# Optimization experiments

Hardware: AMD Instinct MI355X
Metric: run time of the kernel (lower is better)

## Reference

```python
import jax, jax.numpy as jnp
import numpy as np

N_HEAD = 16
EPS = 1e-6


def setup_inputs() -> dict:
    key = jax.random.key(0)
    ks = jax.random.split(key, 5)
    B, T, C = 2, 2048, 1024
    hd = C // N_HEAD
    x = jax.random.normal(ks[0], (B, T, C), dtype=jnp.float32)
    # rotary frequencies (unit-magnitude complex, decomposed into cos/sin)
    theta = 10000.0 ** (-np.arange(0, hd, 2, dtype=np.float32) / hd)  # [hd/2]
    ang = np.arange(T, dtype=np.float32)[:, None] * theta[None, :]    # [T, hd/2]
    freqs_cos = jnp.asarray(np.cos(ang))
    freqs_sin = jnp.asarray(np.sin(ang))
    w_attn = jax.random.normal(ks[1], (3 * C, C), dtype=jnp.float32) * 0.02
    w_proj = jax.random.normal(ks[2], (C, C), dtype=jnp.float32) * 0.02
    q_norm_w = jnp.ones((hd,), dtype=jnp.float32)
    k_norm_w = jnp.ones((hd,), dtype=jnp.float32)
    return {"x": x, "freqs_cos": freqs_cos, "freqs_sin": freqs_sin,
            "w_attn": w_attn, "w_proj": w_proj,
            "q_norm_w": q_norm_w, "k_norm_w": k_norm_w}


def _rmsnorm(x, w):
    # x: [..., hd]; per-last-dim RMSNorm with learned scale
    rms = jax.lax.rsqrt(jnp.mean(x * x, axis=-1, keepdims=True) + EPS)
    return x * rms * w


def _rope(x, cos, sin):
    # x: [B, T, H, hd]; cos/sin: [T, hd/2] -> broadcast [1, T, 1, hd/2]
    x2 = x.reshape(*x.shape[:-1], -1, 2)  # [B,T,H,hd/2,2]
    x0, x1 = x2[..., 0], x2[..., 1]
    c = cos[None, :, None, :]
    s = sin[None, :, None, :]
    r0 = x0 * c - x1 * s
    r1 = x0 * s + x1 * c
    return jnp.stack([r0, r1], axis=-1).reshape(x.shape)


def reference(x, freqs_cos, freqs_sin, w_attn, w_proj, q_norm_w, k_norm_w):
    B, T, C = x.shape
    H = N_HEAD
    hd = C // H
    qkv = x @ w_attn.T  # [B, T, 3C]
    q, k, v = jnp.split(qkv, 3, axis=-1)
    q = q.reshape(B, T, H, hd)
    k = k.reshape(B, T, H, hd)
    v = v.reshape(B, T, H, hd)
    q = _rmsnorm(q, q_norm_w)
    k = _rmsnorm(k, k_norm_w)
    q = _rope(q, freqs_cos[:T], freqs_sin[:T])
    k = _rope(k, freqs_cos[:T], freqs_sin[:T])
    scale = 1.0 / jnp.sqrt(jnp.asarray(hd, dtype=x.dtype))
    # causal SDPA: scores [B, H, T, T]
    scores = jnp.einsum('bihd,bjhd->bhij', q, k) * scale
    causal = jnp.tril(jnp.ones((T, T), dtype=bool))
    scores = jnp.where(causal[None, None], scores, jnp.finfo(scores.dtype).min)
    p = jax.nn.softmax(scores, axis=-1)
    y = jnp.einsum('bhij,bjhd->bihd', p, v).reshape(B, T, C)
    return y @ w_proj.T
```

## Files before the change

kernel.cpp:

```cpp
#include <hip/hip_runtime.h>

typedef unsigned short u16;
typedef unsigned int u32;
typedef __bf16 bf16x8 __attribute__((ext_vector_type(8)));
typedef float f32x4 __attribute__((ext_vector_type(4)));

__device__ __forceinline__ u16 f2bf(float f) {
    union { float f; u32 u; } v;
    v.f = f;
    u32 r = v.u + 0x7fffu + ((v.u >> 16) & 1u);
    return (u16)(r >> 16);
}

__device__ __forceinline__ u32 fbits(float f) {
    union { float f; u32 u; } v; v.f = f; return v.u;
}

__device__ __forceinline__ void glds16(const void* g, void* l) {
    __builtin_amdgcn_global_load_lds(
        (__attribute__((address_space(1))) unsigned int*)(g),
        (__attribute__((address_space(3))) unsigned int*)(l), 16, 0, 0);
}

#define MFMA __builtin_amdgcn_mfma_f32_16x16x32_bf16

__global__ void castbf3(const float* __restrict__ a, u16* __restrict__ oa,
                        const float* __restrict__ b, u16* __restrict__ ob,
                        const float* __restrict__ c, u16* __restrict__ oc,
                        const float* __restrict__ fcos, const float* __restrict__ fsin,
                        float2* __restrict__ csb) {
    int blk = blockIdx.x;
    if (blk < 4096) {
        int i = blk * 256 + threadIdx.x;
        float4 v = ((const float4*)a)[i];
        ushort4 o;
        o.x = f2bf(v.x); o.y = f2bf(v.y); o.z = f2bf(v.z); o.w = f2bf(v.w);
        ((ushort4*)oa)[i] = o;
    } else if (blk < 7168) {
        int i = (blk - 4096) * 256 + threadIdx.x;
        int n = i >> 8, c4 = i & 255;
        int np;
        if (n < 2048) {
            int part = n >> 10, rem = n & 1023;
            int h = rem >> 6, d = rem & 63;
            int nd = (d >> 1) + ((d & 1) << 5);
            np = part * 1024 + h * 64 + nd;
        } else np = n;
        float4 v = ((const float4*)b)[i];
        ushort4 o;
        o.x = f2bf(v.x); o.y = f2bf(v.y); o.z = f2bf(v.z); o.w = f2bf(v.w);
        ((ushort4*)ob)[np * 256 + c4] = o;
    } else if (blk < 8192) {
        int i = (blk - 7168) * 256 + threadIdx.x;
        float4 v = ((const float4*)c)[i];
        ushort4 o;
        o.x = f2bf(v.x); o.y = f2bf(v.y); o.z = f2bf(v.z); o.w = f2bf(v.w);
        ((ushort4*)oc)[i] = o;
    } else {
        int i = (blk - 8192) * 256 + threadIdx.x;
        csb[i] = make_float2(fcos[i], fsin[i]);
    }
}

__global__ __launch_bounds__(256) void gemm_qkv(
    const u16* __restrict__ A, const u16* __restrict__ B,
    const float2* __restrict__ csb,
    const float* __restrict__ qw, const float* __restrict__ kw,
    u16* __restrict__ q, u16* __restrict__ k, u16* __restrict__ vt)
{
    __shared__ alignas(16) u16 As[128 * 32];
    __shared__ alignas(16) u16 Bs[128 * 32];
    __shared__ alignas(16) u16 Es[2 * 128 * 64];
    const int tid = threadIdx.x;
    const int lane = tid & 63;
    const int wave = tid >> 6;
    const int bm = blockIdx.y * 128, bn = blockIdx.x * 128;
    const int wm = (wave >> 1) * 64, wn = (wave & 1) * 64;
    const int ln = lane & 15, quad = lane >> 4;
    const int K = 1024;

    f32x4 acc[4][4] = {};

    const int srow = tid >> 2;
    const int scol = (tid & 3) * 8;
    const u16* gA = A + (size_t)(bm + srow) * K + scol;
    const u16* gB = B + (size_t)(bn + srow) * K + scol;
    u16* lA = &As[wave * 512];
    u16* lB = &Bs[wave * 512];

    for (int k0 = 0; k0 < K; k0 += 32) {
        glds16(gA + k0, lA);
        glds16(gA + (size_t)64 * K + k0, lA + 2048);
        glds16(gB + k0, lB);
        glds16(gB + (size_t)64 * K + k0, lB + 2048);
        __builtin_amdgcn_s_waitcnt(0);
        __syncthreads();

        bf16x8 af[4], bfr[4];
#pragma unroll
        for (int i = 0; i < 4; ++i)
            af[i] = *(const bf16x8*)&As[(wm + i * 16 + ln) * 32 + quad * 8];
#pragma unroll
        for (int j = 0; j < 4; ++j)
            bfr[j] = *(const bf16x8*)&Bs[(wn + j * 16 + ln) * 32 + quad * 8];
#pragma unroll
        for (int i = 0; i < 4; ++i)
#pragma unroll
            for (int j = 0; j < 4; ++j)
                acc[i][j] = MFMA(af[i], bfr[j], acc[i][j], 0, 0, 0);
        __syncthreads();
    }

    const int part = bn >> 10;
    const int headw = wave & 1;
    const int h0 = (bn & 1023) >> 6;
    const float SC = 0.18033688011112042f;
    const int b = bm >> 11, tbase = bm & 2047;

    if (part == 2) {
#pragma unroll
        for (int i = 0; i < 4; ++i) {
            int tlb = wm + i * 16 + quad * 4;
#pragma unroll
            for (int j = 0; j < 4; ++j) {
                int d = j * 16 + ln;
                uint2 pk;
                pk.x = __builtin_amdgcn_perm(fbits(acc[i][j][1]), fbits(acc[i][j][0]), 0x07060302u);
                pk.y = __builtin_amdgcn_perm(fbits(acc[i][j][3]), fbits(acc[i][j][2]), 0x07060302u);
                *(uint2*)&Es[headw * 8192 + d * 128 + (tlb ^ (ln << 3))] = pk;
            }
        }
        __syncthreads();
#pragma unroll
        for (int c = 0; c < 8; ++c) {
            int cid = c * 256 + tid;
            int tc = cid & 15, d = (cid >> 4) & 63, hd = cid >> 10;
            uint4 v = *(const uint4*)&Es[hd * 8192 + d * 128 + ((tc ^ (d & 15)) << 3)];
            size_t dst = ((size_t)((b * 16 + h0 + hd) * 64 + d)) * 2048
                       + tbase + ((tc >> 3) << 6) + (((tc & 7) ^ (d & 7)) << 3);
            *(uint4*)&vt[dst] = v;
        }
        return;
    }

    const float* nw = (part == 0) ? qw : kw;
    float wv[4];
#pragma unroll
    for (int j = 0; j < 4; ++j) {
        int nd = j * 16 + ln;
        int od = ((nd & 31) << 1) | (nd >> 5);
        wv[j] = nw[od];
    }

    if (part == 0) {
#pragma unroll
        for (int i = 0; i < 4; ++i) {
            float oj[4][4];
#pragma unroll
            for (int r = 0; r < 4; ++r) {
                int tloc = wm + i * 16 + quad * 4 + r;
                int t = (bm + tloc) & 2047;
                float v0 = acc[i][0][r], v1 = acc[i][1][r];
                float v2 = acc[i][2][r], v3 = acc[i][3][r];
                float ss = v0 * v0 + v1 * v1 + v2 * v2 + v3 * v3;
                ss += __shfl_xor(ss, 1);
                ss += __shfl_xor(ss, 2);
                ss += __shfl_xor(ss, 4);
                ss += __shfl_xor(ss, 8);
                float g = rsqrtf(ss * (1.0f / 64.0f) + 1e-6f) * SC;
                float x0a = v0 * g * wv[0], x0b = v1 * g * wv[1];
                float x1a = v2 * g * wv[2], x1b = v3 * g * wv[3];
                float2 cs0 = csb[t * 32 + ln];
                float2 cs1 = csb[t * 32 + 16 + ln];
                oj[0][r] = x0a * cs0.x - x1a * cs0.y;
                oj[2][r] = x0a * cs0.y + x1a * cs0.x;
                oj[1][r] = x0b * cs1.x - x1b * cs1.y;
                oj[3][r] = x0b * cs1.y + x1b * cs1.x;
            }
            int tlb = wm + i * 16 + quad * 4;
#pragma unroll
            for (int j = 0; j < 4; ++j) {
                uint2 pk;
                pk.x = __builtin_amdgcn_perm(fbits(oj[j][1]), fbits(oj[j][0]), 0x07060302u);
                pk.y = __builtin_amdgcn_perm(fbits(oj[j][3]), fbits(oj[j][2]), 0x07060302u);
                *(uint2*)&Es[headw * 8192 + (j * 16 + ln) * 128 + (tlb ^ (ln << 3))] = pk;
            }
        }
        __syncthreads();
#pragma unroll
        for (int c = 0; c < 8; ++c) {
            int cid = c * 256 + tid;
            int tc = cid & 15, d = (cid >> 4) & 63, hd = cid >> 10;
            uint4 v = *(const uint4*)&Es[hd * 8192 + d * 128 + ((tc ^ (d & 15)) << 3)];
            size_t dst = ((size_t)((b * 16 + h0 + hd) * 64 + d)) * 2048 + tbase + tc * 8;
            *(uint4*)&q[dst] = v;
        }
        return;
    }

#pragma unroll
    for (int i = 0; i < 4; ++i) {
#pragma unroll
        for (int r = 0; r < 4; ++r) {
            int tloc = wm + i * 16 + quad * 4 + r;
            int t = (bm + tloc) & 2047;

            float v0 = acc[i][0][r], v1 = acc[i][1][r];
            float v2 = acc[i][2][r], v3 = acc[i][3][r];
            float ss = v0 * v0 + v1 * v1 + v2 * v2 + v3 * v3;
            ss += __shfl_xor(ss, 1);
            ss += __shfl_xor(ss, 2);
            ss += __shfl_xor(ss, 4);
            ss += __shfl_xor(ss, 8);
            float g = rsqrtf(ss * (1.0f / 64.0f) + 1e-6f);

            float x0a = v0 * g * wv[0], x0b = v1 * g * wv[1];
            float x1a = v2 * g * wv[2], x1b = v3 * g * wv[3];
            float2 cs0 = csb[t * 32 + ln];
            float2 cs1 = csb[t * 32 + 16 + ln];
            float o0 = x0a * cs0.x - x1a * cs0.y;
            float o2 = x0a * cs0.y + x1a * cs0.x;
            float o1 = x0b * cs1.x - x1b * cs1.y;
            float o3 = x0b * cs1.y + x1b * cs1.x;

            u16* e = &Es[headw * 8192 + tloc * 64 + ln];
            e[((0 ^ quad) << 4)] = f2bf(o0);
            e[((1 ^ quad) << 4)] = f2bf(o1);
            e[((2 ^ quad) << 4)] = f2bf(o2);
            e[((3 ^ quad) << 4)] = f2bf(o3);
        }
    }
    __syncthreads();
#pragma unroll
    for (int c = 0; c < 8; ++c) {
        int cid = c * 256 + tid;
        int dc = cid & 7, tloc = (cid >> 3) & 127, hd = cid >> 10;
        int q2 = (tloc >> 2) & 3;
        int sq = (dc >> 1) ^ q2;
        uint4 v = *(const uint4*)&Es[hd * 8192 + tloc * 64 + sq * 16 + (dc & 1) * 8];
        int gm = bm + tloc;
        int bb = gm >> 11, t = gm & 2047;
        size_t rb = ((size_t)((bb * 16 + h0 + hd) * 2048 + t)) * 64;
        *(uint4*)&k[rb + ((dc ^ (t & 7)) << 3)] = v;
    }
}

__global__ __launch_bounds__(256) void gemm64(
    const u16* __restrict__ A, const u16* __restrict__ B,
    float* __restrict__ C, int M, int N, int K)
{
    __shared__ alignas(16) u16 As[64 * 32];
    __shared__ alignas(16) u16 Bs[128 * 32];
    const int tid = threadIdx.x;
    const int lane = tid & 63;
    const int wave = tid >> 6;
    const int bm = blockIdx.y * 64, bn = blockIdx.x * 128;
    const int wm = (wave >> 1) * 32, wn = (wave & 1) * 64;
    const int ln = lane & 15, quad = lane >> 4;

    f32x4 acc[2][4] = {};

    const int srow = tid >> 2;
    const int scol = (tid & 3) * 8;
    const u16* gA = A + (size_t)(bm + (srow & 63)) * K + scol;
    const u16* gB = B + (size_t)(bn + srow) * K + scol;
    u16* lA = &As[wave * 512];
    u16* lB = &Bs[wave * 512];

    for (int k0 = 0; k0 < K; k0 += 32) {
        glds16(gA + k0, lA);
        glds16(gB + k0, lB);
        glds16(gB + (size_t)64 * K + k0, lB + 2048);
        __builtin_amdgcn_s_waitcnt(0);
        __syncthreads();

        bf16x8 af[2], bfr[4];
#pragma unroll
        for (int i = 0; i < 2; ++i)
            af[i] = *(const bf16x8*)&As[(wm + i * 16 + ln) * 32 + quad * 8];
#pragma unroll
        for (int j = 0; j < 4; ++j)
            bfr[j] = *(const bf16x8*)&Bs[(wn + j * 16 + ln) * 32 + quad * 8];
#pragma unroll
        for (int i = 0; i < 2; ++i)
#pragma unroll
            for (int j = 0; j < 4; ++j)
                acc[i][j] = MFMA(af[i], bfr[j], acc[i][j], 0, 0, 0);
        __syncthreads();
    }

#pragma unroll
    for (int i = 0; i < 2; ++i) {
#pragma unroll
        for (int r = 0; r < 4; ++r) {
            int gm = bm + wm + i * 16 + quad * 4 + r;
            float* Crow = C + (size_t)gm * N + bn + wn + ln;
#pragma unroll
            for (int j = 0; j < 4; ++j)
                Crow[j * 16] = acc[i][j][r];
        }
    }
}

__global__ __launch_bounds__(512) void attn_kernel(
    const u16* __restrict__ Q, const u16* __restrict__ K,
    const u16* __restrict__ VT, u16* __restrict__ Y)
{
    __shared__ alignas(16) u16 Ks[2][64 * 64];
    __shared__ alignas(16) u16 Vs[2][64 * 64];
    __shared__ alignas(16) u16 Ps[8][16 * 80];

    const int tid = threadIdx.x;
    const int lane = tid & 63;
    const int wave = tid >> 6;
    const int ln = lane & 15, quad = lane >> 4;
    const int pi = blockIdx.x;
    const int bh = blockIdx.y;
    const int qaIdx = pi, qbIdx = 31 - pi;
    const bool isB = wave >= 4;
    const int qidx = isB ? qbIdx : qaIdx;
    const int myq = qidx * 64 + (wave & 3) * 16;
    const size_t base = (size_t)bh * 2048 * 64;
    const u16* Kg = K + base;
    const u16* Vg = VT + base;
    const __bf16* Qg = (const __bf16*)(Q + base);

    const int qt = myq + ln;
    bf16x8 qf0, qf1;
#pragma unroll
    for (int j = 0; j < 8; ++j) {
        qf0[j] = Qg[(size_t)(quad * 8 + j) * 2048 + qt];
        qf1[j] = Qg[(size_t)(32 + quad * 8 + j) * 2048 + qt];
    }

    f32x4 o[4] = {};
    float l = 0.0f;
    const int nstages = qbIdx + 1;
    const int sw = ln & 7;
    const int srow = wave * 8 + (lane >> 3);
    const int scol = (lane & 7) * 8;
    u16* Psw = &Ps[wave][0];

    auto prefetch = [&](int jb, int nb) {
        glds16(&Kg[(size_t)(jb + srow) * 64 + scol], &Ks[nb][wave * 512]);
        glds16(&Vg[(size_t)srow * 2048 + jb + scol], &Vs[nb][wave * 512]);
    };
    prefetch(0, 0);

    for (int jt = 0; jt < nstages; ++jt) {
        const int jbn = (jt + 1 < nstages) ? (jt + 1) * 64 : 0;
        prefetch(jbn, (jt + 1) & 1);
        asm volatile("s_waitcnt vmcnt(2)\n\ts_barrier" ::: "memory");

        const u16* ksb = &Ks[jt & 1][0];
        const u16* vsb = &Vs[jt & 1][0];

        if (isB || jt <= qaIdx) {
            f32x4 st[4];
#pragma unroll
            for (int ct = 0; ct < 4; ++ct) {
                bf16x8 kf0 = *(const bf16x8*)&ksb[(ct * 16 + ln) * 64 + ((0 + quad) ^ sw) * 8];
                bf16x8 kf1 = *(const bf16x8*)&ksb[(ct * 16 + ln) * 64 + ((4 + quad) ^ sw) * 8];
                f32x4 z = {};
                z = MFMA(kf0, qf0, z, 0, 0, 0);
                st[ct] = MFMA(kf1, qf1, z, 0, 0, 0);
            }
            if (jt == qidx) {
                const int qg = myq + ln;
                const int jb = jt * 64;
#pragma unroll
                for (int ct = 0; ct < 4; ++ct)
#pragma unroll
                    for (int r = 0; r < 4; ++r)
                        if (jb + ct * 16 + quad * 4 + r > qg) st[ct][r] = -1e30f;
            }

            float sum = 0.0f;
#pragma unroll
            for (int ct = 0; ct < 4; ++ct) {
                float e0 = exp2f(st[ct][0]), e1 = exp2f(st[ct][1]);
                float e2 = exp2f(st[ct][2]), e3 = exp2f(st[ct][3]);
                sum += (e0 + e1) + (e2 + e3);
                uint2 pk;
                pk.x = __builtin_amdgcn_perm(fbits(e1), fbits(e0), 0x07060302u);
                pk.y = __builtin_amdgcn_perm(fbits(e3), fbits(e2), 0x07060302u);
                *(uint2*)&Psw[ln * 80 + ct * 16 + quad * 4] = pk;
            }
            sum += __shfl_xor(sum, 16);
            sum += __shfl_xor(sum, 32);
            l += sum;

            __builtin_amdgcn_s_waitcnt(0xC07F);
            bf16x8 pf0 = *(const bf16x8*)&Psw[ln * 80 + quad * 8];
            bf16x8 pf1 = *(const bf16x8*)&Psw[ln * 80 + 32 + quad * 8];

#pragma unroll
            for (int dt = 0; dt < 4; ++dt) {
                bf16x8 vf0 = *(const bf16x8*)&vsb[(dt * 16 + ln) * 64 + ((0 + quad) ^ sw) * 8];
                bf16x8 vf1 = *(const bf16x8*)&vsb[(dt * 16 + ln) * 64 + ((4 + quad) ^ sw) * 8];
                o[dt] = MFMA(pf0, vf0, o[dt], 0, 0, 0);
                o[dt] = MFMA(pf1, vf1, o[dt], 0, 0, 0);
            }
        }
        asm volatile("s_waitcnt lgkmcnt(0)\n\ts_barrier" ::: "memory");
    }

    const int b = bh >> 4, h = bh & 15;
#pragma unroll
    for (int r = 0; r < 4; ++r) {
        float lr = __shfl(l, (lane & 48) + quad * 4 + r);
        float inv = 1.0f / lr;
        int gq = myq + quad * 4 + r;
        size_t yb = ((size_t)(b * 2048 + gq)) * 1024 + h * 64 + ln;
#pragma unroll
        for (int dt = 0; dt < 4; ++dt)
            Y[yb + dt * 16] = f2bf(o[dt][r] * inv);
    }
}

extern "C" void kernel_launch(void* const* d_in, const int* in_sizes, int n_in,
                              void* d_out, int out_size, void* d_ws, size_t ws_size,
                              hipStream_t stream) {
    const float* x      = (const float*)d_in[0];
    const float* fcos   = (const float*)d_in[1];
    const float* fsin   = (const float*)d_in[2];
    const float* w_attn = (const float*)d_in[3];
    const float* w_proj = (const float*)d_in[4];
    const float* qw     = (const float*)d_in[5];
    const float* kw     = (const float*)d_in[6];
    float* out = (float*)d_out;

    char* ws = (char*)d_ws;
    u16*    xb  = (u16*)(ws + 0);
    u16*    yb  = (u16*)(ws + 0);
    u16*    wab = (u16*)(ws + 8388608);
    u16*    wpb = (u16*)(ws + 14680064);
    u16*    qb  = (u16*)(ws + 16777216);
    u16*    kb  = (u16*)(ws + 25165824);
    u16*    vtb = (u16*)(ws + 33554432);
    float2* csb = (float2*)(ws + 41943040);

    castbf3<<<8448, 256, 0, stream>>>(x, xb, w_attn, wab, w_proj, wpb, fcos, fsin, csb);

    gemm_qkv<<<dim3(24, 32), 256, 0, stream>>>(xb, wab, csb, qw, kw, qb, kb, vtb);

    attn_kernel<<<dim3(16, 32), 512, 0, stream>>>(qb, kb, vtb, yb);

    gemm64<<<dim3(8, 64), 256, 0, stream>>>(yb, wpb, out, 4096, 1024, 1024);
}
```

Measured before the change: 206.7 us.

## Double-buffer LDS tiles in QKV and projection GEMMs to overlap loads

Both GEMM kernels now keep two LDS stages and issue the global-to-LDS loads for the next K tile before computing on the current one. They wait with a partial vmcnt instead of draining every load each iteration. The goal is to hide global memory latency behind the MFMA work. The QKV GEMM reuses its epilogue buffer for the stages, which adds a final drain and barrier. The last iteration issues a redundant wraparound load, and gemm64 now hard-codes 32 K iterations and changes the A row mapping, which is valid only for K=1024.

```diff
diff --git a/kernel.cpp b/kernel.cpp
--- a/kernel.cpp
+++ b/kernel.cpp
@@ -68,9 +68,8 @@
     const float* __restrict__ qw, const float* __restrict__ kw,
     u16* __restrict__ q, u16* __restrict__ k, u16* __restrict__ vt)
 {
-    __shared__ alignas(16) u16 As[128 * 32];
-    __shared__ alignas(16) u16 Bs[128 * 32];
-    __shared__ alignas(16) u16 Es[2 * 128 * 64];
+    __shared__ alignas(16) u16 SB[2 * 8192];
+    u16* Es = SB;
     const int tid = threadIdx.x;
     const int lane = tid & 63;
     const int wave = tid >> 6;
@@ -85,31 +84,39 @@
     const int scol = (tid & 3) * 8;
     const u16* gA = A + (size_t)(bm + srow) * K + scol;
     const u16* gB = B + (size_t)(bn + srow) * K + scol;
-    u16* lA = &As[wave * 512];
-    u16* lB = &Bs[wave * 512];
-
-    for (int k0 = 0; k0 < K; k0 += 32) {
+
+    auto stage = [&](int k0, int bf) {
+        u16* lA = &SB[bf * 8192 + wave * 512];
+        u16* lB = &SB[bf * 8192 + 4096 + wave * 512];
         glds16(gA + k0, lA);
         glds16(gA + (size_t)64 * K + k0, lA + 2048);
         glds16(gB + k0, lB);
         glds16(gB + (size_t)64 * K + k0, lB + 2048);
-        __builtin_amdgcn_s_waitcnt(0);
-        __syncthreads();
-
+    };
+
+    stage(0, 0);
+    for (int it = 0; it < 32; ++it) {
+        stage((((it + 1) & 31) << 5), (it + 1) & 1);
+        asm volatile("s_waitcnt vmcnt(4)\n\ts_barrier" ::: "memory");
+
+        const u16* Asb = &SB[(it & 1) * 8192];
+        const u16* Bsb = Asb + 4096;
         bf16x8 af[4], bfr[4];
 #pragma unroll
         for (int i = 0; i < 4; ++i)
-            af[i] = *(const bf16x8*)&As[(wm + i * 16 + ln) * 32 + quad * 8];
+            af[i] = *(const bf16x8*)&Asb[(wm + i * 16 + ln) * 32 + quad * 8];
 #pragma unroll
         for (int j = 0; j < 4; ++j)
-            bfr[j] = *(const bf16x8*)&Bs[(wn + j * 16 + ln) * 32 + quad * 8];
+            bfr[j] = *(const bf16x8*)&Bsb[(wn + j * 16 + ln) * 32 + quad * 8];
 #pragma unroll
         for (int i = 0; i < 4; ++i)
 #pragma unroll
             for (int j = 0; j < 4; ++j)
                 acc[i][j] = MFMA(af[i], bfr[j], acc[i][j], 0, 0, 0);
-        __syncthreads();
-    }
+
+        asm volatile("s_barrier" ::: "memory");
+    }
+    asm volatile("s_waitcnt vmcnt(0)\n\ts_barrier" ::: "memory");
 
     const int part = bn >> 10;
     const int headw = wave & 1;
@@ -249,8 +256,7 @@
     const u16* __restrict__ A, const u16* __restrict__ B,
     float* __restrict__ C, int M, int N, int K)
 {
-    __shared__ alignas(16) u16 As[64 * 32];
-    __shared__ alignas(16) u16 Bs[128 * 32];
+    __shared__ alignas(16) u16 SB[2 * 6144];
     const int tid = threadIdx.x;
     const int lane = tid & 63;
     const int wave = tid >> 6;
@@ -262,31 +268,38 @@
 
     const int srow = tid >> 2;
     const int scol = (tid & 3) * 8;
-    const u16* gA = A + (size_t)(bm + (srow & 63)) * K + scol;
+    const u16* gA = A + (size_t)(bm + srow) * K + scol;
     const u16* gB = B + (size_t)(bn + srow) * K + scol;
-    u16* lA = &As[wave * 512];
-    u16* lB = &Bs[wave * 512];
-
-    for (int k0 = 0; k0 < K; k0 += 32) {
+
+    auto stage = [&](int k0, int bf) {
+        u16* lA = &SB[bf * 6144 + wave * 512];
+        u16* lB = &SB[bf * 6144 + 2048 + wave * 512];
         glds16(gA + k0, lA);
         glds16(gB + k0, lB);
         glds16(gB + (size_t)64 * K + k0, lB + 2048);
-        __builtin_amdgcn_s_waitcnt(0);
-        __syncthreads();
-
+    };
+
+    stage(0, 0);
+    for (int it = 0; it < 32; ++it) {
+        stage((((it + 1) & 31) << 5), (it + 1) & 1);
+        asm volatile("s_waitcnt vmcnt(3)\n\ts_barrier" ::: "memory");
+
+        const u16* Asb = &SB[(it & 1) * 6144];
+        const u16* Bsb = Asb + 2048;
         bf16x8 af[2], bfr[4];
 #pragma unroll
         for (int i = 0; i < 2; ++i)
-            af[i] = *(const bf16x8*)&As[(wm + i * 16 + ln) * 32 + quad * 8];
+            af[i] = *(const bf16x8*)&Asb[(wm + i * 16 + ln) * 32 + quad * 8];
 #pragma unroll
         for (int j = 0; j < 4; ++j)
-            bfr[j] = *(const bf16x8*)&Bs[(wn + j * 16 + ln) * 32 + quad * 8];
+            bfr[j] = *(const bf16x8*)&Bsb[(wn + j * 16 + ln) * 32 + quad * 8];
 #pragma unroll
         for (int i = 0; i < 2; ++i)
 #pragma unroll
             for (int j = 0; j < 4; ++j)
                 acc[i][j] = MFMA(af[i], bfr[j], acc[i][j], 0, 0, 0);
-        __syncthreads();
+
+        asm volatile("s_barrier" ::: "memory");
     }
 
 #pragma unroll
```

Result: faster. 193.0 us (-6.6%).
